# Kernel optimization log

Measured on AMD Instinct MI355X. Metric: run time of the kernel, lower is better.

The kernel has to match this reference:

```python
import jax, jax.numpy as jnp
import numpy as np
import math

CHUNK = 64

def _linear(x, W, b):
    # torch nn.Linear: y = x @ W.T + b
    return jnp.einsum('bsd,ed->bse', x, W) + b

def setup_inputs() -> dict:
    key = jax.random.key(0)
    ks = jax.random.split(key, 10)
    B, S, D = 4, 4096, 512
    scale = 0.02
    inp = {
        'x': jax.random.normal(ks[0], (B, S, D), jnp.float32),
        'base_phases': jax.random.normal(ks[1], (S, D), jnp.float32) * math.pi,
        'Wk': jax.random.normal(ks[2], (D, D), jnp.float32) * scale,
        'bk': jnp.zeros((D,), jnp.float32),
        'Wv': jax.random.normal(ks[3], (D, D), jnp.float32) * scale,
        'bv': jnp.zeros((D,), jnp.float32),
        'Wq': jax.random.normal(ks[4], (D, D), jnp.float32) * scale,
        'bq': jnp.zeros((D,), jnp.float32),
        'Wkm': jax.random.normal(ks[5], (D, D), jnp.float32) * scale,
        'bkm': jnp.zeros((D,), jnp.float32),
        'Wqm': jax.random.normal(ks[6], (D, D), jnp.float32) * scale,
        'bqm': jnp.zeros((D,), jnp.float32),
        'mod_scale': jnp.ones((1,), jnp.float32) * 0.1,
        'ln_g': jnp.ones((D,), jnp.float32),
        'ln_b': jnp.zeros((D,), jnp.float32),
        'Wo': jax.random.normal(ks[7], (D, D), jnp.float32) * scale,
        'bo': jnp.zeros((D,), jnp.float32),
    }
    return inp

def reference(x, base_phases, Wk, bk, Wv, bv, Wq, bq, Wkm, bkm, Wqm, bqm, mod_scale, ln_g, ln_b, Wo, bo):
    B, S, D = x.shape
    bp = base_phases[:S][None]                      # [1,S,D]
    key = _linear(x, Wk, bk)
    value = _linear(x, Wv, bv)
    query = _linear(x, Wq, bq)
    key_phase = bp + _linear(key, Wkm, bkm) * mod_scale
    query_phase = bp + _linear(query, Wqm, bqm) * mod_scale
    bound_real = value * jnp.cos(key_phase)
    bound_imag = value * jnp.sin(key_phase)
    # chunked cumulative memory (S divisible by CHUNK -> no padding)
    nC = S // CHUNK
    br = bound_real.reshape(B, nC, CHUNK, D)
    bi = bound_imag.reshape(B, nC, CHUNK, D)
    qp = query_phase.reshape(B, nC, CHUNK, D)
    mem_real = jnp.cumsum(br, axis=2)
    mem_imag = jnp.cumsum(bi, axis=2)
    retrieved = (mem_real * jnp.cos(qp) + mem_imag * jnp.sin(qp)).reshape(B, S, D)
    retrieved = retrieved / math.sqrt(D)
    # LayerNorm + Linear (to_out)
    mu = jnp.mean(retrieved, axis=-1, keepdims=True)
    var = jnp.mean((retrieved - mu) ** 2, axis=-1, keepdims=True)
    normed = (retrieved - mu) / jnp.sqrt(var + 1e-5) * ln_g + ln_b
    out = _linear(normed, Wo, bo)
    return x + out
```

## Files before the change

### kernel.cpp

```cpp
#include <hip/hip_runtime.h>
#include <hip/hip_bf16.h>


typedef __attribute__((ext_vector_type(8))) short short8;
typedef __attribute__((ext_vector_type(4))) float f32x4;

#define M_TOK   16384
#define DIM     512
#define NCHUNK  64
#define RPAD    520

__device__ __forceinline__ void gll16(const void* g, void* l) {
  __builtin_amdgcn_global_load_lds(
      (const __attribute__((address_space(1))) unsigned int*)g,
      (__attribute__((address_space(3))) unsigned int*)l, 16, 0, 0);
}

__device__ __forceinline__ uint2 pack4bf(float4 v) {
  union { __hip_bfloat16 h[4]; uint2 u; } t;
  t.h[0] = __float2bfloat16(v.x);
  t.h[1] = __float2bfloat16(v.y);
  t.h[2] = __float2bfloat16(v.z);
  t.h[3] = __float2bfloat16(v.w);
  return t.u;
}

__global__ __launch_bounds__(256) void prep_all(
    const float* __restrict__ x, __hip_bfloat16* __restrict__ x_bf,
    const float* __restrict__ Wv, const float* __restrict__ Wo,
    const float* __restrict__ bv,
    const float* __restrict__ Wkm, const float* __restrict__ Wqm,
    const float* __restrict__ Wk, const float* __restrict__ Wq,
    const float* __restrict__ bk, const float* __restrict__ bkm,
    const float* __restrict__ bq, const float* __restrict__ bqm,
    __hip_bfloat16* __restrict__ Wall, float* __restrict__ bc1,
    __hip_bfloat16* __restrict__ Wm_bf, __hip_bfloat16* __restrict__ WT_bf) {
  const int tid = threadIdx.x;
  if (blockIdx.x < 8192) {
    int i = blockIdx.x * 256 + tid;
    ((uint2*)x_bf)[i] = pack4bf(((const float4*)x)[i]);
    return;
  }
  const int b = blockIdx.x - 8192;
  if (b < 512) {
    int m = b >> 8;
    int idx = ((b & 255) * 256 + tid) * 4;
    const float* src = m ? Wo : Wv;
    __hip_bfloat16* dst = Wall + (m ? (size_t)1536 * 512 : 0);
    ((uint2*)dst)[idx >> 2] = pack4bf(*(const float4*)(src + idx));
    int t = b * 256 + tid;
    if (t < 512) bc1[t] = bv[t];
  } else if (b < 1024) {
    int bb = b - 512;
    int m = bb >> 8;
    int idx = ((bb & 255) * 256 + tid) * 4;
    const float* src = m ? Wqm : Wkm;
    ((uint2*)(Wm_bf + (size_t)m * 262144))[idx >> 2] =
        pack4bf(*(const float4*)(src + idx));
  } else if (b < 1152) {
    __shared__ float tile[64][65];
    int bb = b - 1024;
    int z = bb >> 6;
    int tl = bb & 63;
    int tr = tl >> 3, tc = tl & 7;
    const float* src = z ? Wq : Wk;
#pragma unroll
    for (int i = 0; i < 4; i++) {
      int r = (tid >> 4) + 16 * i;
      int c4 = (tid & 15) * 4;
      float4 v = *(const float4*)(src + (size_t)(tr * 64 + r) * 512 +
                                  tc * 64 + c4);
      tile[r][c4 + 0] = v.x;
      tile[r][c4 + 1] = v.y;
      tile[r][c4 + 2] = v.z;
      tile[r][c4 + 3] = v.w;
    }
    __syncthreads();
    int orow = tid >> 2;
    int seg = tid & 3;
    __hip_bfloat16* dst = WT_bf + (size_t)z * 262144 +
                          (size_t)(tc * 64 + orow) * 512 + tr * 64 + seg * 16;
#pragma unroll
    for (int q = 0; q < 4; q++) {
      float4 v;
      v.x = tile[seg * 16 + q * 4 + 0][orow];
      v.y = tile[seg * 16 + q * 4 + 1][orow];
      v.z = tile[seg * 16 + q * 4 + 2][orow];
      v.w = tile[seg * 16 + q * 4 + 3][orow];
      *(uint2*)(dst + q * 4) = pack4bf(v);
    }
  } else {
    int row = (b - 1152) * 4 + (tid >> 6);
    int lane = tid & 63;
    int z = row >> 9;
    int i = row & 511;
    const float* Wm = z ? Wqm : Wkm;
    const float* b0 = z ? bq : bk;
    const float* bm = z ? bqm : bkm;
    const float4* w4 = (const float4*)(Wm + (size_t)i * 512 + lane * 8);
    const float4* v4 = (const float4*)(b0 + lane * 8);
    float4 w0 = w4[0], w1 = w4[1], c0 = v4[0], c1 = v4[1];
    float acc = w0.x * c0.x + w0.y * c0.y + w0.z * c0.z + w0.w * c0.w +
                w1.x * c1.x + w1.y * c1.y + w1.z * c1.z + w1.w * c1.w;
#pragma unroll
    for (int off = 32; off; off >>= 1) acc += __shfl_xor(acc, off, 64);
    if (lane == 0) bc1[512 + z * 512 + i] = acc + bm[i];
  }
}

__global__ __launch_bounds__(256) void gemm_bt(
    const __hip_bfloat16* __restrict__ A, int lda,
    const __hip_bfloat16* __restrict__ Bt,
    const float* __restrict__ bias,
    __hip_bfloat16* __restrict__ Cout, int ldc) {
  constexpr int K = 512, BK = 32;
  __shared__ __align__(16) __hip_bfloat16 As[128 * BK];
  __shared__ __align__(16) __hip_bfloat16 Bs[128 * BK];

  const int tid  = threadIdx.x;
  const int lane = tid & 63;
  const int w    = tid >> 6;
  const int wm   = w >> 1;
  const int wn   = w & 1;
  const int m0   = blockIdx.y * 128;
  const int n0   = blockIdx.x * 128;

  const int rS0    = (w * 2 + 0) * 16 + (lane >> 2);
  const int rS1    = (w * 2 + 1) * 16 + (lane >> 2);
  const int kInRow = (lane & 3) * 8;
  const __hip_bfloat16* gA0 = A + (size_t)(m0 + rS0) * lda + kInRow;
  const __hip_bfloat16* gA1 = A + (size_t)(m0 + rS1) * lda + kInRow;
  const __hip_bfloat16* gB0 = Bt + (size_t)(n0 + rS0) * K + kInRow;
  const __hip_bfloat16* gB1 = Bt + (size_t)(n0 + rS1) * K + kInRow;
  char* ldsA0 = (char*)As + (w * 2 + 0) * 1024;
  char* ldsA1 = (char*)As + (w * 2 + 1) * 1024;
  char* ldsB0 = (char*)Bs + (w * 2 + 0) * 1024;
  char* ldsB1 = (char*)Bs + (w * 2 + 1) * 1024;

  f32x4 acc[4][4] = {};

  const int rfA = lane & 15;
  const int rfK = (lane >> 4) * 8;

  for (int kt = 0; kt < K; kt += BK) {
    __syncthreads();
    gll16(gA0 + kt, ldsA0);
    gll16(gA1 + kt, ldsA1);
    gll16(gB0 + kt, ldsB0);
    gll16(gB1 + kt, ldsB1);
    __syncthreads();

    short8 af[4], bf[4];
#pragma unroll
    for (int i = 0; i < 4; i++)
      af[i] = *(const short8*)(As + (wm * 64 + i * 16 + rfA) * BK + rfK);
#pragma unroll
    for (int j = 0; j < 4; j++)
      bf[j] = *(const short8*)(Bs + (wn * 64 + j * 16 + rfA) * BK + rfK);
#pragma unroll
    for (int i = 0; i < 4; i++)
#pragma unroll
      for (int j = 0; j < 4; j++)
        acc[i][j] = __builtin_amdgcn_mfma_f32_16x16x32_bf16(
            af[i], bf[j], acc[i][j], 0, 0, 0);
  }

  const int cq = lane >> 4;
#pragma unroll
  for (int i = 0; i < 4; i++) {
    int row = m0 + wm * 64 + i * 16 + cq * 4;
#pragma unroll
    for (int j = 0; j < 4; j++) {
      int col = n0 + wn * 64 + j * 16 + (lane & 15);
      float bz = bias[col];
#pragma unroll
      for (int r = 0; r < 4; r++) {
        float v = acc[i][j][r] + bz;
        Cout[(size_t)(row + r) * ldc + col] = __float2bfloat16(v);
      }
    }
  }
}

__global__ __launch_bounds__(256) void gemm_compose(
    const __hip_bfloat16* __restrict__ Wm_bf,
    const __hip_bfloat16* __restrict__ WT_bf,
    __hip_bfloat16* __restrict__ Wall) {
  constexpr int K = 512, BK = 32;
  const __hip_bfloat16* A  = Wm_bf + (size_t)blockIdx.z * 262144;
  const __hip_bfloat16* Bt = WT_bf + (size_t)blockIdx.z * 262144;
  __hip_bfloat16* C = Wall + (size_t)(512 + blockIdx.z * 512) * 512;
  __shared__ __align__(16) __hip_bfloat16 As[128 * BK];
  __shared__ __align__(16) __hip_bfloat16 Bs[128 * BK];

  const int tid  = threadIdx.x;
  const int lane = tid & 63;
  const int w    = tid >> 6;
  const int wm   = w >> 1;
  const int wn   = w & 1;
  const int m0   = blockIdx.y * 128;
  const int n0   = blockIdx.x * 128;

  const int rS0    = (w * 2 + 0) * 16 + (lane >> 2);
  const int rS1    = (w * 2 + 1) * 16 + (lane >> 2);
  const int kInRow = (lane & 3) * 8;
  const __hip_bfloat16* gA0 = A + (size_t)(m0 + rS0) * K + kInRow;
  const __hip_bfloat16* gA1 = A + (size_t)(m0 + rS1) * K + kInRow;
  const __hip_bfloat16* gB0 = Bt + (size_t)(n0 + rS0) * K + kInRow;
  const __hip_bfloat16* gB1 = Bt + (size_t)(n0 + rS1) * K + kInRow;
  char* ldsA0 = (char*)As + (w * 2 + 0) * 1024;
  char* ldsA1 = (char*)As + (w * 2 + 1) * 1024;
  char* ldsB0 = (char*)Bs + (w * 2 + 0) * 1024;
  char* ldsB1 = (char*)Bs + (w * 2 + 1) * 1024;

  f32x4 acc[4][4] = {};
  const int rfA = lane & 15;
  const int rfK = (lane >> 4) * 8;

  for (int kt = 0; kt < K; kt += BK) {
    __syncthreads();
    gll16(gA0 + kt, ldsA0);
    gll16(gA1 + kt, ldsA1);
    gll16(gB0 + kt, ldsB0);
    gll16(gB1 + kt, ldsB1);
    __syncthreads();

    short8 af[4], bf[4];
#pragma unroll
    for (int i = 0; i < 4; i++)
      af[i] = *(const short8*)(As + (wm * 64 + i * 16 + rfA) * BK + rfK);
#pragma unroll
    for (int j = 0; j < 4; j++)
      bf[j] = *(const short8*)(Bs + (wn * 64 + j * 16 + rfA) * BK + rfK);
#pragma unroll
    for (int i = 0; i < 4; i++)
#pragma unroll
      for (int j = 0; j < 4; j++)
        acc[i][j] = __builtin_amdgcn_mfma_f32_16x16x32_bf16(
            af[i], bf[j], acc[i][j], 0, 0, 0);
  }

  const int cq = lane >> 4;
#pragma unroll
  for (int i = 0; i < 4; i++) {
    int row = m0 + wm * 64 + i * 16 + cq * 4;
#pragma unroll
    for (int j = 0; j < 4; j++) {
      int col = n0 + wn * 64 + j * 16 + (lane & 15);
#pragma unroll
      for (int r = 0; r < 4; r++)
        C[(size_t)(row + r) * 512 + col] = __float2bfloat16(acc[i][j][r]);
    }
  }
}

__global__ __launch_bounds__(1024) void fused_pg(
    const __hip_bfloat16* __restrict__ VKQ,
    const float* __restrict__ bp,
    const float* __restrict__ mod_scale,
    const float* __restrict__ ln_g, const float* __restrict__ ln_b,
    const __hip_bfloat16* __restrict__ WoB,
    const float* __restrict__ bo,
    const float* __restrict__ x,
    float* __restrict__ out) {
  __shared__ __hip_bfloat16 R[64 * RPAD];
  __shared__ float Tr[512], Ti[512];
  const int tid    = threadIdx.x;
  const int seg    = tid >> 9;
  const int d      = tid & 511;
  const int blk    = blockIdx.x;
  const int token0 = blk * 64;
  const int sg0    = (blk & (NCHUNK - 1)) * 64;
  const float msc  = mod_scale[0];
  const float isd  = 0.044194173824159216f;

  {
    const int s0 = seg * 32;
    float mr = 0.f, mi = 0.f;
    const __hip_bfloat16* vb = VKQ + (size_t)(token0 + s0) * 1536 + d;
    const float* bb = bp + (size_t)(sg0 + s0) * 512 + d;
#pragma unroll 4
    for (int s = 0; s < 32; ++s) {
      float v  = __bfloat162float(vb[(size_t)s * 1536]);
      float km = __bfloat162float(vb[(size_t)s * 1536 + 512]);
      float qm = __bfloat162float(vb[(size_t)s * 1536 + 1024]);
      float b  = bb[(size_t)s * 512];
      float kp = b + km * msc;
      float qp = b + qm * msc;
      float sk, ck, sq, cq;
      __sincosf(kp, &sk, &ck);
      __sincosf(qp, &sq, &cq);
      mr += v * ck;
      mi += v * sk;
      R[(s0 + s) * RPAD + d] = __float2bfloat16((mr * cq + mi * sq) * isd);
    }
    if (seg == 0) {
      Tr[d] = mr;
      Ti[d] = mi;
    }
  }
  __syncthreads();

  {
    const int r0 = 32 + seg * 16;
    const float pr = Tr[d] * isd;
    const float pi = Ti[d] * isd;
    const __hip_bfloat16* qb = VKQ + (size_t)(token0 + r0) * 1536 + 1024 + d;
    const float* bb = bp + (size_t)(sg0 + r0) * 512 + d;
#pragma unroll 4
    for (int s = 0; s < 16; ++s) {
      float qm = __bfloat162float(qb[(size_t)s * 1536]);
      float b  = bb[(size_t)s * 512];
      float qp = b + qm * msc;
      float sq, cq;
      __sincosf(qp, &sq, &cq);
      int idx = (r0 + s) * RPAD + d;
      float v = __bfloat162float(R[idx]) + pr * cq + pi * sq;
      R[idx] = __float2bfloat16(v);
    }
  }
  __syncthreads();

  {
    const int lane = tid & 63;
    const int wv   = tid >> 6;
    float gj[8], bj[8];
#pragma unroll
    for (int j = 0; j < 8; j++) {
      int col = lane + 64 * j;
      gj[j] = ln_g[col];
      bj[j] = ln_b[col];
    }
    for (int rr = 0; rr < 4; ++rr) {
      int row = wv * 4 + rr;
      float vals[8], sum = 0.f, sq2 = 0.f;
#pragma unroll
      for (int j = 0; j < 8; j++) {
        float v = __bfloat162float(R[row * RPAD + lane + 64 * j]);
        vals[j] = v;
        sum += v;
        sq2 += v * v;
      }
#pragma unroll
      for (int off = 32; off; off >>= 1) {
        sum += __shfl_xor(sum, off, 64);
        sq2 += __shfl_xor(sq2, off, 64);
      }
      float mu   = sum * (1.f / 512.f);
      float var  = sq2 * (1.f / 512.f) - mu * mu;
      float rstd = rsqrtf(var + 1e-5f);
#pragma unroll
      for (int j = 0; j < 8; j++) {
        float nv = (vals[j] - mu) * rstd * gj[j] + bj[j];
        R[row * RPAD + lane + 64 * j] = __float2bfloat16(nv);
      }
    }
  }
  __syncthreads();

  {
    const int lane = tid & 63;
    const int w    = tid >> 6;
    const int rfA  = lane & 15;
    const int rfK  = (lane >> 4) * 8;
    f32x4 acc[4][2] = {};

    for (int kt = 0; kt < 512; kt += 32) {
      short8 af[4], bf[2];
#pragma unroll
      for (int j = 0; j < 2; j++) {
        int col = w * 32 + j * 16 + rfA;
        bf[j] = *(const short8*)(WoB + (size_t)col * 512 + kt + rfK);
      }
#pragma unroll
      for (int i = 0; i < 4; i++)
        af[i] = *(const short8*)(R + (i * 16 + rfA) * RPAD + kt + rfK);
#pragma unroll
      for (int i = 0; i < 4; i++)
#pragma unroll
        for (int j = 0; j < 2; j++)
          acc[i][j] = __builtin_amdgcn_mfma_f32_16x16x32_bf16(
              af[i], bf[j], acc[i][j], 0, 0, 0);
    }

    const int cq = lane >> 4;
    float bz[2];
#pragma unroll
    for (int j = 0; j < 2; j++) bz[j] = bo[w * 32 + j * 16 + (lane & 15)];
#pragma unroll
    for (int i = 0; i < 4; i++) {
      int row = token0 + i * 16 + cq * 4;
#pragma unroll
      for (int j = 0; j < 2; j++) {
        int col = w * 32 + j * 16 + (lane & 15);
#pragma unroll
        for (int r = 0; r < 4; r++) {
          size_t o = (size_t)(row + r) * 512 + col;
          out[o] = acc[i][j][r] + bz[j] + x[o];
        }
      }
    }
  }
}

extern "C" void kernel_launch(void* const* d_in, const int* in_sizes, int n_in,
                              void* d_out, int out_size, void* d_ws,
                              size_t ws_size, hipStream_t stream) {
  const float* x    = (const float*)d_in[0];
  const float* bp   = (const float*)d_in[1];
  const float* Wk   = (const float*)d_in[2];
  const float* bk   = (const float*)d_in[3];
  const float* Wv   = (const float*)d_in[4];
  const float* bv   = (const float*)d_in[5];
  const float* Wq   = (const float*)d_in[6];
  const float* bq   = (const float*)d_in[7];
  const float* Wkm  = (const float*)d_in[8];
  const float* bkm  = (const float*)d_in[9];
  const float* Wqm  = (const float*)d_in[10];
  const float* bqm  = (const float*)d_in[11];
  const float* msc  = (const float*)d_in[12];
  const float* lng  = (const float*)d_in[13];
  const float* lnb  = (const float*)d_in[14];
  const float* Wo   = (const float*)d_in[15];
  const float* bo   = (const float*)d_in[16];
  float* out = (float*)d_out;

  char* ws = (char*)d_ws;
  __hip_bfloat16* x_bf  = (__hip_bfloat16*)ws;  ws += (size_t)M_TOK * DIM * 2;
  __hip_bfloat16* Wall  = (__hip_bfloat16*)ws;  ws += (size_t)2048 * 512 * 2;
  __hip_bfloat16* Wm_bf = (__hip_bfloat16*)ws;  ws += (size_t)2 * 262144 * 2;
  __hip_bfloat16* WT_bf = (__hip_bfloat16*)ws;  ws += (size_t)2 * 262144 * 2;
  float*          bc1   = (float*)ws;           ws += 1536 * 4;
  __hip_bfloat16* VKQ   = (__hip_bfloat16*)ws;  ws += (size_t)M_TOK * 1536 * 2;

  prep_all<<<9600, 256, 0, stream>>>(x, x_bf, Wv, Wo, bv, Wkm, Wqm, Wk, Wq,
                                     bk, bkm, bq, bqm, Wall, bc1, Wm_bf,
                                     WT_bf);
  gemm_compose<<<dim3(4, 4, 2), 256, 0, stream>>>(Wm_bf, WT_bf, Wall);
  gemm_bt<<<dim3(12, 128), 256, 0, stream>>>(x_bf, DIM, Wall, bc1, VKQ, 1536);
  fused_pg<<<256, 1024, 0, stream>>>(VKQ, bp, msc, lng, lnb,
                                     Wall + (size_t)1536 * 512, bo, x, out);
}
```

Before: 206.5 us.

## Widen GEMM k-step, swizzle block order, restructure chunk scan into four segments

The projection GEMM now loads two K-slices per barrier pair, which halves the number of syncs. It also remaps the 1D grid so that consecutive blocks are spread across XCD-like groups, aiming at better L2 locality. The fused phase kernel now has each thread handle two adjacent dims with vectorized loads over four 16-row segments, and it caches the query sin/cos values in registers instead of recomputing them in the carry pass. It also prefetches the x residual before the LayerNorm so that latency overlaps. These changes raise register pressure (64 cached trig floats plus 32 x values at 1024 threads) and may cause spills.

```diff
diff --git a/kernel.cpp b/kernel.cpp
--- a/kernel.cpp
+++ b/kernel.cpp
@@ -23,6 +23,19 @@
   t.h[2] = __float2bfloat16(v.z);
   t.h[3] = __float2bfloat16(v.w);
   return t.u;
+}
+
+__device__ __forceinline__ unsigned int pack2bf(float a, float b) {
+  union { __hip_bfloat16 h[2]; unsigned int u; } t;
+  t.h[0] = __float2bfloat16(a);
+  t.h[1] = __float2bfloat16(b);
+  return t.u;
+}
+
+__device__ __forceinline__ float u2f(unsigned short u) {
+  union { unsigned int i; float f; } t;
+  t.i = (unsigned int)u << 16;
+  return t.f;
 }
 
 __global__ __launch_bounds__(256) void prep_all(
@@ -114,16 +127,19 @@
     const float* __restrict__ bias,
     __hip_bfloat16* __restrict__ Cout, int ldc) {
   constexpr int K = 512, BK = 32;
-  __shared__ __align__(16) __hip_bfloat16 As[128 * BK];
-  __shared__ __align__(16) __hip_bfloat16 Bs[128 * BK];
+  __shared__ __align__(16) __hip_bfloat16 As[2][128 * BK];
+  __shared__ __align__(16) __hip_bfloat16 Bs[2][128 * BK];
 
   const int tid  = threadIdx.x;
   const int lane = tid & 63;
   const int w    = tid >> 6;
   const int wm   = w >> 1;
   const int wn   = w & 1;
-  const int m0   = blockIdx.y * 128;
-  const int n0   = blockIdx.x * 128;
+  const int lb = (blockIdx.x & 7) * 192 + (blockIdx.x >> 3);
+  const int by = lb / 12;
+  const int bx = lb - by * 12;
+  const int m0 = by * 128;
+  const int n0 = bx * 128;
 
   const int rS0    = (w * 2 + 0) * 16 + (lane >> 2);
   const int rS1    = (w * 2 + 1) * 16 + (lane >> 2);
@@ -132,37 +148,46 @@
   const __hip_bfloat16* gA1 = A + (size_t)(m0 + rS1) * lda + kInRow;
   const __hip_bfloat16* gB0 = Bt + (size_t)(n0 + rS0) * K + kInRow;
   const __hip_bfloat16* gB1 = Bt + (size_t)(n0 + rS1) * K + kInRow;
-  char* ldsA0 = (char*)As + (w * 2 + 0) * 1024;
-  char* ldsA1 = (char*)As + (w * 2 + 1) * 1024;
-  char* ldsB0 = (char*)Bs + (w * 2 + 0) * 1024;
-  char* ldsB1 = (char*)Bs + (w * 2 + 1) * 1024;
+  char* ldsA0 = (char*)&As[0][0] + (w * 2 + 0) * 1024;
+  char* ldsA1 = (char*)&As[0][0] + (w * 2 + 1) * 1024;
+  char* ldsB0 = (char*)&Bs[0][0] + (w * 2 + 0) * 1024;
+  char* ldsB1 = (char*)&Bs[0][0] + (w * 2 + 1) * 1024;
 
   f32x4 acc[4][4] = {};
 
   const int rfA = lane & 15;
   const int rfK = (lane >> 4) * 8;
 
-  for (int kt = 0; kt < K; kt += BK) {
+  for (int kt = 0; kt < K; kt += 2 * BK) {
     __syncthreads();
     gll16(gA0 + kt, ldsA0);
     gll16(gA1 + kt, ldsA1);
     gll16(gB0 + kt, ldsB0);
     gll16(gB1 + kt, ldsB1);
+    gll16(gA0 + kt + BK, ldsA0 + 8192);
+    gll16(gA1 + kt + BK, ldsA1 + 8192);
+    gll16(gB0 + kt + BK, ldsB0 + 8192);
+    gll16(gB1 + kt + BK, ldsB1 + 8192);
     __syncthreads();
 
-    short8 af[4], bf[4];
-#pragma unroll
-    for (int i = 0; i < 4; i++)
-      af[i] = *(const short8*)(As + (wm * 64 + i * 16 + rfA) * BK + rfK);
-#pragma unroll
-    for (int j = 0; j < 4; j++)
-      bf[j] = *(const short8*)(Bs + (wn * 64 + j * 16 + rfA) * BK + rfK);
-#pragma unroll
-    for (int i = 0; i < 4; i++)
+#pragma unroll
+    for (int h = 0; h < 2; h++) {
+      const __hip_bfloat16* Ah = &As[h][0];
+      const __hip_bfloat16* Bh = &Bs[h][0];
+      short8 af[4], bfv[4];
+#pragma unroll
+      for (int i = 0; i < 4; i++)
+        af[i] = *(const short8*)(Ah + (wm * 64 + i * 16 + rfA) * BK + rfK);
 #pragma unroll
       for (int j = 0; j < 4; j++)
-        acc[i][j] = __builtin_amdgcn_mfma_f32_16x16x32_bf16(
-            af[i], bf[j], acc[i][j], 0, 0, 0);
+        bfv[j] = *(const short8*)(Bh + (wn * 64 + j * 16 + rfA) * BK + rfK);
+#pragma unroll
+      for (int i = 0; i < 4; i++)
+#pragma unroll
+        for (int j = 0; j < 4; j++)
+          acc[i][j] = __builtin_amdgcn_mfma_f32_16x16x32_bf16(
+              af[i], bfv[j], acc[i][j], 0, 0, 0);
+    }
   }
 
   const int cq = lane >> 4;
@@ -264,66 +289,85 @@
     const float* __restrict__ x,
     float* __restrict__ out) {
   __shared__ __hip_bfloat16 R[64 * RPAD];
-  __shared__ float Tr[512], Ti[512];
+  __shared__ float Tr[3][512], Ti[3][512];
   const int tid    = threadIdx.x;
-  const int seg    = tid >> 9;
-  const int d      = tid & 511;
+  const int seg    = tid >> 8;
+  const int d0     = (tid & 255) * 2;
   const int blk    = blockIdx.x;
   const int token0 = blk * 64;
   const int sg0    = (blk & (NCHUNK - 1)) * 64;
   const float msc  = mod_scale[0];
   const float isd  = 0.044194173824159216f;
 
+  float cqs0[16], sqs0[16], cqs1[16], sqs1[16];
+
   {
-    const int s0 = seg * 32;
-    float mr = 0.f, mi = 0.f;
-    const __hip_bfloat16* vb = VKQ + (size_t)(token0 + s0) * 1536 + d;
-    const float* bb = bp + (size_t)(sg0 + s0) * 512 + d;
-#pragma unroll 4
-    for (int s = 0; s < 32; ++s) {
-      float v  = __bfloat162float(vb[(size_t)s * 1536]);
-      float km = __bfloat162float(vb[(size_t)s * 1536 + 512]);
-      float qm = __bfloat162float(vb[(size_t)s * 1536 + 1024]);
-      float b  = bb[(size_t)s * 512];
-      float kp = b + km * msc;
-      float qp = b + qm * msc;
-      float sk, ck, sq, cq;
-      __sincosf(kp, &sk, &ck);
-      __sincosf(qp, &sq, &cq);
-      mr += v * ck;
-      mi += v * sk;
-      R[(s0 + s) * RPAD + d] = __float2bfloat16((mr * cq + mi * sq) * isd);
-    }
-    if (seg == 0) {
-      Tr[d] = mr;
-      Ti[d] = mi;
+    const int r0 = seg * 16;
+    float mr0 = 0.f, mi0 = 0.f, mr1 = 0.f, mi1 = 0.f;
+    const __hip_bfloat16* vb = VKQ + (size_t)(token0 + r0) * 1536 + d0;
+    const float* bb = bp + (size_t)(sg0 + r0) * 512 + d0;
+#pragma unroll
+    for (int s = 0; s < 16; ++s) {
+      ushort2 v2  = *(const ushort2*)(vb + (size_t)s * 1536);
+      ushort2 km2 = *(const ushort2*)(vb + (size_t)s * 1536 + 512);
+      ushort2 qm2 = *(const ushort2*)(vb + (size_t)s * 1536 + 1024);
+      float2 b2   = *(const float2*)(bb + (size_t)s * 512);
+      float v0 = u2f((unsigned short)v2.x), v1 = u2f((unsigned short)v2.y);
+      float kp0 = b2.x + u2f((unsigned short)km2.x) * msc;
+      float kp1 = b2.y + u2f((unsigned short)km2.y) * msc;
+      float qp0 = b2.x + u2f((unsigned short)qm2.x) * msc;
+      float qp1 = b2.y + u2f((unsigned short)qm2.y) * msc;
+      float sk0, ck0, sk1, ck1, sq0, cq0, sq1, cq1;
+      __sincosf(kp0, &sk0, &ck0);
+      __sincosf(kp1, &sk1, &ck1);
+      __sincosf(qp0, &sq0, &cq0);
+      __sincosf(qp1, &sq1, &cq1);
+      mr0 += v0 * ck0; mi0 += v0 * sk0;
+      mr1 += v1 * ck1; mi1 += v1 * sk1;
+      cqs0[s] = cq0; sqs0[s] = sq0;
+      cqs1[s] = cq1; sqs1[s] = sq1;
+      float rr0 = (mr0 * cq0 + mi0 * sq0) * isd;
+      float rr1 = (mr1 * cq1 + mi1 * sq1) * isd;
+      *(unsigned int*)(&R[(r0 + s) * RPAD + d0]) = pack2bf(rr0, rr1);
+    }
+    if (seg < 3) {
+      Tr[seg][d0] = mr0; Tr[seg][d0 + 1] = mr1;
+      Ti[seg][d0] = mi0; Ti[seg][d0 + 1] = mi1;
     }
   }
   __syncthreads();
 
+  if (seg) {
+    float pr0 = Tr[0][d0],     pi0 = Ti[0][d0];
+    float pr1 = Tr[0][d0 + 1], pi1 = Ti[0][d0 + 1];
+    if (seg >= 2) {
+      pr0 += Tr[1][d0];     pi0 += Ti[1][d0];
+      pr1 += Tr[1][d0 + 1]; pi1 += Ti[1][d0 + 1];
+    }
+    if (seg == 3) {
+      pr0 += Tr[2][d0];     pi0 += Ti[2][d0];
+      pr1 += Tr[2][d0 + 1]; pi1 += Ti[2][d0 + 1];
+    }
+    pr0 *= isd; pi0 *= isd; pr1 *= isd; pi1 *= isd;
+    const int r0 = seg * 16;
+#pragma unroll
+    for (int s = 0; s < 16; ++s) {
+      unsigned int* p = (unsigned int*)(&R[(r0 + s) * RPAD + d0]);
+      unsigned int old = *p;
+      float a = u2f((unsigned short)(old & 0xffffu)) +
+                pr0 * cqs0[s] + pi0 * sqs0[s];
+      float b = u2f((unsigned short)(old >> 16)) +
+                pr1 * cqs1[s] + pi1 * sqs1[s];
+      *p = pack2bf(a, b);
+    }
+  }
+  __syncthreads();
+
+  const int lane = tid & 63;
+  const int wv   = tid >> 6;
+  float xv[4][2][4];
+
   {
-    const int r0 = 32 + seg * 16;
-    const float pr = Tr[d] * isd;
-    const float pi = Ti[d] * isd;
-    const __hip_bfloat16* qb = VKQ + (size_t)(token0 + r0) * 1536 + 1024 + d;
-    const float* bb = bp + (size_t)(sg0 + r0) * 512 + d;
-#pragma unroll 4
-    for (int s = 0; s < 16; ++s) {
-      float qm = __bfloat162float(qb[(size_t)s * 1536]);
-      float b  = bb[(size_t)s * 512];
-      float qp = b + qm * msc;
-      float sq, cq;
-      __sincosf(qp, &sq, &cq);
-      int idx = (r0 + s) * RPAD + d;
-      float v = __bfloat162float(R[idx]) + pr * cq + pi * sq;
-      R[idx] = __float2bfloat16(v);
-    }
-  }
-  __syncthreads();
-
-  {
-    const int lane = tid & 63;
-    const int wv   = tid >> 6;
     float gj[8], bj[8];
 #pragma unroll
     for (int j = 0; j < 8; j++) {
@@ -331,12 +375,24 @@
       gj[j] = ln_g[col];
       bj[j] = ln_b[col];
     }
+    {
+      const int cq_ = lane >> 4;
+      const int c0  = lane & 15;
+#pragma unroll
+      for (int i = 0; i < 4; i++)
+#pragma unroll
+        for (int j = 0; j < 2; j++)
+#pragma unroll
+          for (int r = 0; r < 4; r++)
+            xv[i][j][r] = x[(size_t)(token0 + i * 16 + cq_ * 4 + r) * 512 +
+                            wv * 32 + j * 16 + c0];
+    }
     for (int rr = 0; rr < 4; ++rr) {
       int row = wv * 4 + rr;
       float vals[8], sum = 0.f, sq2 = 0.f;
 #pragma unroll
       for (int j = 0; j < 8; j++) {
-        float v = __bfloat162float(R[row * RPAD + lane + 64 * j]);
+        float v = u2f(*(const unsigned short*)&R[row * RPAD + lane + 64 * j]);
         vals[j] = v;
         sum += v;
         sq2 += v * v;
@@ -359,18 +415,16 @@
   __syncthreads();
 
   {
-    const int lane = tid & 63;
-    const int w    = tid >> 6;
-    const int rfA  = lane & 15;
-    const int rfK  = (lane >> 4) * 8;
+    const int rfA = lane & 15;
+    const int rfK = (lane >> 4) * 8;
     f32x4 acc[4][2] = {};
 
     for (int kt = 0; kt < 512; kt += 32) {
-      short8 af[4], bf[2];
+      short8 af[4], bfv[2];
 #pragma unroll
       for (int j = 0; j < 2; j++) {
-        int col = w * 32 + j * 16 + rfA;
-        bf[j] = *(const short8*)(WoB + (size_t)col * 512 + kt + rfK);
+        int col = wv * 32 + j * 16 + rfA;
+        bfv[j] = *(const short8*)(WoB + (size_t)col * 512 + kt + rfK);
       }
 #pragma unroll
       for (int i = 0; i < 4; i++)
@@ -380,23 +434,23 @@
 #pragma unroll
         for (int j = 0; j < 2; j++)
           acc[i][j] = __builtin_amdgcn_mfma_f32_16x16x32_bf16(
-              af[i], bf[j], acc[i][j], 0, 0, 0);
-    }
-
-    const int cq = lane >> 4;
+              af[i], bfv[j], acc[i][j], 0, 0, 0);
+    }
+
+    const int cq_ = lane >> 4;
     float bz[2];
 #pragma unroll
-    for (int j = 0; j < 2; j++) bz[j] = bo[w * 32 + j * 16 + (lane & 15)];
+    for (int j = 0; j < 2; j++) bz[j] = bo[wv * 32 + j * 16 + (lane & 15)];
 #pragma unroll
     for (int i = 0; i < 4; i++) {
-      int row = token0 + i * 16 + cq * 4;
+      int row = token0 + i * 16 + cq_ * 4;
 #pragma unroll
       for (int j = 0; j < 2; j++) {
-        int col = w * 32 + j * 16 + (lane & 15);
+        int col = wv * 32 + j * 16 + (lane & 15);
 #pragma unroll
         for (int r = 0; r < 4; r++) {
           size_t o = (size_t)(row + r) * 512 + col;
-          out[o] = acc[i][j][r] + bz[j] + x[o];
+          out[o] = acc[i][j][r] + bz[j] + xv[i][j][r];
         }
       }
     }
@@ -437,7 +491,7 @@
                                      bk, bkm, bq, bqm, Wall, bc1, Wm_bf,
                                      WT_bf);
   gemm_compose<<<dim3(4, 4, 2), 256, 0, stream>>>(Wm_bf, WT_bf, Wall);
-  gemm_bt<<<dim3(12, 128), 256, 0, stream>>>(x_bf, DIM, Wall, bc1, VKQ, 1536);
+  gemm_bt<<<dim3(1536), 256, 0, stream>>>(x_bf, DIM, Wall, bc1, VKQ, 1536);
   fused_pg<<<256, 1024, 0, stream>>>(VKQ, bp, msc, lng, lnb,
                                      Wall + (size_t)1536 * 512, bo, x, out);
 }
```

Result: faster. 202.3 us (-2.0%).
